# Kernel optimization log

Hardware: AMD Instinct MI355X
Metric: run time of the kernel (lower is better)

The kernel has to match this reference:

```python
import jax, jax.numpy as jnp
import numpy as np

B, N, X_DIM, Y_DIM, H_DIM, R_DIM = 64, 512, 128, 128, 4096, 1024


def setup_inputs() -> dict:
    key = jax.random.key(0)
    ks = jax.random.split(key, 10)
    x = jax.random.normal(ks[0], (B, N, X_DIM), dtype=jnp.float32)
    y = jax.random.normal(ks[1], (B, N, Y_DIM), dtype=jnp.float32)
    # per-sample context lengths in [1, N]; prefix mask guarantees >=1 True per row
    lengths = jax.random.randint(ks[2], (B,), 1, N + 1)
    mask = (jnp.arange(N)[None, :] < lengths[:, None])  # [B, N] bool
    d_in = X_DIM + Y_DIM
    s1 = 1.0 / np.sqrt(d_in)
    s2 = 1.0 / np.sqrt(H_DIM)
    W1 = jax.random.uniform(ks[3], (d_in, H_DIM), jnp.float32, -s1, s1)
    b1 = jax.random.uniform(ks[4], (H_DIM,), jnp.float32, -s1, s1)
    W2 = jax.random.uniform(ks[5], (H_DIM, H_DIM), jnp.float32, -s2, s2)
    b2 = jax.random.uniform(ks[6], (H_DIM,), jnp.float32, -s2, s2)
    W3 = jax.random.uniform(ks[7], (H_DIM, R_DIM), jnp.float32, -s2, s2)
    b3 = jax.random.uniform(ks[8], (R_DIM,), jnp.float32, -s2, s2)
    return {"x": x, "y": y, "mask": mask,
            "W1": W1, "b1": b1, "W2": W2, "b2": b2, "W3": W3, "b3": b3}


def reference(x, y, mask, W1, b1, W2, b2, W3, b3):
    # Dense equivalent of gather -> MLP -> scatter_mean by batch id:
    # the MLP is pointwise over tokens, so applying it densely and taking a
    # masked mean over the point dim gives identical math to the ragged path.
    nn_in = jnp.concatenate([x, y], axis=-1)          # [B, N, x+y]
    h = jax.nn.relu(jnp.einsum('bnd,dh->bnh', nn_in, W1) + b1)
    h = jax.nn.relu(jnp.einsum('bnh,hk->bnk', h, W2) + b2)
    r = jnp.einsum('bnk,kr->bnr', h, W3) + b3          # [B, N, r_dim]
    m = mask.astype(r.dtype)[..., None]                # [B, N, 1]
    counts = jnp.maximum(m.sum(axis=1), 1.0)           # [B, 1]
    r_aggr = (r * m).sum(axis=1) / counts              # [B, r_dim]
    return r_aggr
```

## Files before the change

### kernel.cpp

```cpp
#include <hip/hip_runtime.h>


using u16 = unsigned short;
using u8 = unsigned char;
typedef float f32x4 __attribute__((ext_vector_type(4)));
typedef short s16x8 __attribute__((ext_vector_type(8)));
typedef int i32x4 __attribute__((ext_vector_type(4)));

__device__ __forceinline__ u16 f2bf(float f) {
  union { float f; unsigned u; } v; v.f = f;
  unsigned r = (v.u + 0x7fffu + ((v.u >> 16) & 1u)) >> 16;
  return (u16)r;
}


__global__ void count_k(const int* __restrict__ mask, int* __restrict__ lens) {
  int b = blockIdx.x, l = threadIdx.x;
  const int4* row = (const int4*)(mask + (size_t)b * 512);
  int4 v0 = row[l];
  int4 v1 = row[l + 64];
  int s = v0.x + v0.y + v0.z + v0.w + v1.x + v1.y + v1.z + v1.w;
  #pragma unroll
  for (int o = 32; o; o >>= 1) s += __shfl_down(s, o);
  if (l == 0) lens[b] = s;
}

__global__ void meta_k(const int* __restrict__ lens, int* __restrict__ meta) {
  if (threadIdx.x == 0) {
    int acc = 0; meta[0] = 0;
    for (int b = 0; b < 64; ++b) { acc += lens[b]; meta[b + 1] = acc; }
    meta[65] = acc;
    meta[66] = (acc + 127) >> 7;
  }
}

__global__ void tok2b_k(const int* __restrict__ meta, int* __restrict__ tok2b) {
  int i = blockIdx.x * 256 + threadIdx.x;
  int total = meta[65];
  int b = 64;
  if (i < total) {
    int lo = 0, hi = 64;
    while (hi - lo > 1) { int mid = (lo + hi) >> 1; if (meta[mid] <= i) lo = mid; else hi = mid; }
    b = lo;
  }
  tok2b[i] = b;
}

__global__ void build_a(const float* __restrict__ x, const float* __restrict__ y,
                        const int* __restrict__ meta, const int* __restrict__ tok2b,
                        u16* __restrict__ A) {
  int i4 = blockIdx.x * 256 + threadIdx.x;
  int e = i4 * 4;
  int m = e >> 8, c = e & 255;
  int total = meta[65];
  ushort4 o = {0, 0, 0, 0};
  if (m < total) {
    int b = tok2b[m], t = m - meta[b];
    const float* src = (c < 128) ? x + ((size_t)b * 512 + t) * 128 + c
                                 : y + ((size_t)b * 512 + t) * 128 + (c - 128);
    float4 v = *(const float4*)src;
    o.x = f2bf(v.x); o.y = f2bf(v.y); o.z = f2bf(v.z); o.w = f2bf(v.w);
  }
  *(ushort4*)&A[e] = o;
}

__global__ void pack_k(const float* __restrict__ W, u16* __restrict__ P,
                       int N, int NKB) {
  long c = (long)blockIdx.x * 256 + threadIdx.x;
  int lane = c & 63; long r = c >> 6;
  int s = r & 1; int j = (r >> 1) & 3; int wn = (r >> 3) & 1;
  long q = r >> 4;
  int ktb = (int)(q % NKB), nt = (int)(q / NKB);
  int k = ktb * 64 + s * 32 + (lane >> 4) * 8;
  int n = nt * 128 + wn * 64 + j * 16 + (lane & 15);
  ushort o[8];
  #pragma unroll
  for (int e = 0; e < 8; ++e) o[e] = f2bf(W[(size_t)(k + e) * N + n]);
  *(uint4*)&P[c * 8] = *(uint4*)o;
}

__global__ void colmax_k(const float* __restrict__ W, float* __restrict__ cmax) {
  int n = blockIdx.x * 256 + threadIdx.x;
  int k0 = blockIdx.y * 128;
  float m = 0.f;
  for (int k = k0; k < k0 + 128; ++k)
    m = fmaxf(m, fabsf(W[(size_t)k * 4096 + n]));
  atomicMax((int*)&cmax[n], __float_as_int(m));
}

__global__ void pack8_k(const float* __restrict__ W, const float* __restrict__ cmax,
                        char* __restrict__ P) {
  long c = (long)blockIdx.x * 256 + threadIdx.x;
  int lane = c & 63; long r = c >> 6;
  int j = r & 3; int wn = (r >> 2) & 1; long q = r >> 3;
  int ktb = (int)(q & 63), nt = (int)(q >> 6);
  int k = ktb * 64 + (lane >> 4) * 16;
  int n = nt * 128 + wn * 64 + j * 16 + (lane & 15);
  float rw = 127.0f / fmaxf(cmax[n], 1e-20f);
  char o[16];
  #pragma unroll
  for (int e = 0; e < 16; ++e) {
    int v = __float2int_rn(W[(size_t)(k + e) * 4096 + n] * rw);
    v = v > 127 ? 127 : (v < -127 ? -127 : v);
    o[e] = (char)v;
  }
  *(uint4*)&P[c * 16] = *(const uint4*)o;
}

__global__ void sn_k(const float* __restrict__ S, const int* __restrict__ lens,
                     u16* __restrict__ Sn) {
  int i4 = blockIdx.x * 256 + threadIdx.x;
  int e = i4 * 4;
  int m = e >> 12;
  float inv = (m < 64) ? (1.0f / (float)lens[m]) : 0.0f;
  float4 v = *(const float4*)(S + e);
  ushort4 o;
  o.x = f2bf(v.x * inv); o.y = f2bf(v.y * inv);
  o.z = f2bf(v.z * inv); o.w = f2bf(v.w * inv);
  *(ushort4*)&Sn[e] = o;
}

template <int MODE>
__global__ __launch_bounds__(256, 3) void gemm_k(
    const void* __restrict__ Av, int lda, const void* __restrict__ BPv,
    const float* __restrict__ bias, const float* __restrict__ cmax,
    u8* __restrict__ Hout, float* __restrict__ Sout, float* __restrict__ Fout,
    const int* __restrict__ meta, const int* __restrict__ tok2b,
    int K, int Nld, int tile0, int tile_cap) {
  constexpr bool A8 = (MODE == 1);
  constexpr int WC_STEADY = A8 ? 0x0F7A : 0x0F7C;
  __shared__ union {
    u16 a16[2][128 * 64];
    u8  a8[2][128 * 64];
    u8  outT8[128 * 128];
  } sm;

  const int tid = threadIdx.x;
  const int wave = tid >> 6;
  const int lane = tid & 63;
  const int wm = wave >> 1, wn = wave & 1;
  const int quad = lane >> 4, l15 = lane & 15;
  const int NKB = K >> 6;

  int nslots;
  if constexpr (MODE < 2) {
    int tc = meta[66] - tile0;
    tc = tc < 0 ? 0 : (tc > tile_cap ? tile_cap : tc);
    nslots = tc * 32;
  } else {
    nslots = gridDim.x;
  }

  for (int slot = blockIdx.x; slot < nslots; slot += gridDim.x) {
    int mt, n0, k0, kend;
    if constexpr (MODE < 2) {
      mt = slot >> 5; n0 = (slot & 31) << 7; k0 = 0; kend = K;
    } else {
      mt = 0; n0 = slot << 7; k0 = blockIdx.y * 512; kend = k0 + 512;
    }

    f32x4 accf[4][4];
    i32x4 acci[4][4];
    #pragma unroll
    for (int i = 0; i < 4; i++)
      #pragma unroll
      for (int j = 0; j < 4; j++) {
        if constexpr (A8) acci[i][j] = (i32x4){0, 0, 0, 0};
        else accf[i][j] = (f32x4){0.f, 0.f, 0.f, 0.f};
      }

    const u8* ag8[2];
    const u16* ag16[4];
    if constexpr (A8) {
      #pragma unroll
      for (int il = 0; il < 2; ++il) {
        int ci = (wave * 2 + il) * 64 + lane;
        int m = ci >> 2, c = (ci & 3) ^ ((m >> 1) & 3);
        ag8[il] = (const u8*)Av + (size_t)(mt * 128 + m) * lda + c * 16;
      }
    } else {
      #pragma unroll
      for (int il = 0; il < 4; ++il) {
        int ci = (wave * 4 + il) * 64 + lane;
        int m = ci >> 3, c = (ci & 7) ^ (m & 7);
        ag16[il] = (const u16*)Av + (size_t)(mt * 128 + m) * lda + c * 8;
      }
    }
    const u16* bw = nullptr;
    const u8* bw8 = nullptr;
    if constexpr (A8)
      bw8 = (const u8*)BPv + (size_t)(n0 >> 7) * NKB * 8192 + wn * 4096 + lane * 16;
    else
      bw = (const u16*)BPv + (size_t)(n0 >> 7) * NKB * 8192 + wn * 4096 + lane * 8;

    s16x8 breg0[8], breg1[8];
    i32x4 breg8_0[4], breg8_1[4];

    auto stageA = [&](int kt, int buf) {
      if constexpr (A8) {
        #pragma unroll
        for (int il = 0; il < 2; ++il)
          __builtin_amdgcn_global_load_lds(
              (const __attribute__((address_space(1))) void*)(ag8[il] + kt),
              (__attribute__((address_space(3))) void*)(&sm.a8[buf][(wave * 2 + il) * 1024]),
              16, 0, 0);
      } else {
        #pragma unroll
        for (int il = 0; il < 4; ++il)
          __builtin_amdgcn_global_load_lds(
              (const __attribute__((address_space(1))) void*)(ag16[il] + kt),
              (__attribute__((address_space(3))) void*)(&sm.a16[buf][(wave * 4 + il) * 512]),
              16, 0, 0);
      }
    };
    auto loadB = [&](int kt, int which) {
      if constexpr (A8) {
        i32x4* dst = which ? breg8_1 : breg8_0;
        const u8* p = bw8 + (size_t)(kt >> 6) * 8192;
        #pragma unroll
        for (int j = 0; j < 4; j++)
          dst[j] = *(const i32x4*)(p + j * 1024);
      } else {
        s16x8* dst = which ? breg1 : breg0;
        const u16* p = bw + (size_t)(kt >> 6) * 8192;
        #pragma unroll
        for (int j = 0; j < 4; j++)
          #pragma unroll
          for (int s = 0; s < 2; s++)
            dst[j * 2 + s] = *(const s16x8*)(p + j * 1024 + s * 512);
      }
    };
    auto compute = [&](int buf) {
      if constexpr (A8) {
        const i32x4* br = buf ? breg8_1 : breg8_0;
        #pragma unroll
        for (int i = 0; i < 4; i++) {
          int m = wm * 64 + i * 16 + l15;
          int addr = (m * 4 + (quad ^ ((m >> 1) & 3))) * 16;
          i32x4 a = *(const i32x4*)&sm.a8[buf][addr];
          #pragma unroll
          for (int j = 0; j < 4; j++)
            acci[i][j] = __builtin_amdgcn_mfma_i32_16x16x64_i8(
                a, br[j], acci[i][j], 0, 0, 0);
        }
      } else {
        const s16x8* br = buf ? breg1 : breg0;
        #pragma unroll
        for (int s = 0; s < 2; ++s) {
          s16x8 af[4];
          #pragma unroll
          for (int i = 0; i < 4; i++) {
            int m = wm * 64 + i * 16 + l15;
            int c = (s * 4 + quad) ^ (m & 7);
            af[i] = *(const s16x8*)&sm.a16[buf][(m * 8 + c) * 8];
          }
          #pragma unroll
          for (int i = 0; i < 4; i++)
            #pragma unroll
            for (int j = 0; j < 4; j++)
              accf[i][j] = __builtin_amdgcn_mfma_f32_16x16x32_bf16(
                  af[i], br[j * 2 + s], accf[i][j], 0, 0, 0);
        }
      }
    };

    stageA(k0, 0);
    if (k0 + 64 < kend) stageA(k0 + 64, 1);
    loadB(k0, 0);

    for (int kt = k0; kt < kend; kt += 128) {
      loadB(kt + 64, 1);
      __builtin_amdgcn_s_waitcnt(WC_STEADY);
      __builtin_amdgcn_s_barrier();
      compute(0);
      __builtin_amdgcn_s_barrier();
      if (kt + 128 < kend) stageA(kt + 128, 0);
      if (kt + 128 < kend) {
        loadB(kt + 128, 0);
        __builtin_amdgcn_s_waitcnt(WC_STEADY);
      } else {
        __builtin_amdgcn_s_waitcnt(0x0F70);
      }
      __builtin_amdgcn_s_barrier();
      compute(1);
      __builtin_amdgcn_s_barrier();
      if (kt + 192 < kend) stageA(kt + 192, 1);
    }
    __syncthreads();

    if constexpr (MODE == 0) {
      float bb[4];
      #pragma unroll
      for (int j = 0; j < 4; j++) bb[j] = bias[n0 + wn * 64 + j * 16 + l15];
      #pragma unroll
      for (int i = 0; i < 4; i++)
        #pragma unroll
        for (int j = 0; j < 4; j++) {
          int col = wn * 64 + j * 16 + l15;
          #pragma unroll
          for (int r = 0; r < 4; r++) {
            int row = wm * 64 + i * 16 + quad * 4 + r;
            float v = accf[i][j][r] + bb[j];
            v = v > 0.f ? v : 0.f;
            int qv = (int)(v * 32.0f + 0.5f);
            if (qv > 127) qv = 127;
            sm.outT8[row * 128 + col] = (u8)qv;
          }
        }
      __syncthreads();
      #pragma unroll
      for (int u = 0; u < 4; ++u) {
        int e = u * 256 + tid;
        int row = e >> 3, c16 = (e & 7) * 16;
        *(uint4*)&Hout[(size_t)(mt * 128 + row) * Nld + n0 + c16] =
            *(const uint4*)&sm.outT8[row * 128 + c16];
      }
      __syncthreads();
    } else if constexpr (MODE == 1) {
      float bb[4], sc[4];
      #pragma unroll
      for (int j = 0; j < 4; j++) {
        int col_ = n0 + wn * 64 + j * 16 + l15;
        bb[j] = bias[col_];
        sc[j] = cmax[col_] * (1.0f / (127.0f * 32.0f));
      }
      int tb[16];
      const int gbase = tile0 * 128 + mt * 128 + wm * 64 + quad * 4;
      #pragma unroll
      for (int i = 0; i < 4; i++)
        #pragma unroll
        for (int r = 0; r < 4; r++) tb[i * 4 + r] = tok2b[gbase + i * 16 + r];
      #pragma unroll
      for (int j = 0; j < 4; j++) {
        int col = n0 + wn * 64 + j * 16 + l15;
        float sum = 0.f;
        int cb = tb[0];
        #pragma unroll
        for (int idx = 0; idx < 16; ++idx) {
          float t = (float)acci[idx >> 2][j][idx & 3] * sc[j] + bb[j];
          t = t > 0.f ? t : 0.f;
          int b = tb[idx];
          if (b != cb) {
            atomicAdd(&Sout[(size_t)cb * 4096 + col], sum);
            sum = 0.f; cb = b;
          }
          sum += t;
        }
        atomicAdd(&Sout[(size_t)cb * 4096 + col], sum);
      }
    } else {
      float bb[4];
      #pragma unroll
      for (int j = 0; j < 4; j++)
        bb[j] = (blockIdx.y == 0) ? bias[n0 + wn * 64 + j * 16 + l15] : 0.f;
      #pragma unroll
      for (int i = 0; i < 4; i++)
        #pragma unroll
        for (int j = 0; j < 4; j++) {
          int col = wn * 64 + j * 16 + l15;
          #pragma unroll
          for (int r = 0; r < 4; r++) {
            int row = wm * 64 + i * 16 + quad * 4 + r;
            if (row < 64)
              atomicAdd(&Fout[(size_t)row * Nld + n0 + col], accf[i][j][r] + bb[j]);
          }
        }
    }
  }
}

extern "C" void kernel_launch(void* const* d_in, const int* in_sizes, int n_in,
                              void* d_out, int out_size, void* d_ws, size_t ws_size,
                              hipStream_t stream) {
  const float* x  = (const float*)d_in[0];
  const float* y  = (const float*)d_in[1];
  const int* mask = (const int*)d_in[2];
  const float* W1 = (const float*)d_in[3];
  const float* b1 = (const float*)d_in[4];
  const float* W2 = (const float*)d_in[5];
  const float* b2 = (const float*)d_in[6];
  const float* W3 = (const float*)d_in[7];
  const float* b3 = (const float*)d_in[8];
  float* out = (float*)d_out;

  char* ws = (char*)d_ws;
  size_t off = 0;
  auto alloc = [&](size_t bytes) {
    char* p = ws + off;
    off += (bytes + 255) & ~(size_t)255;
    return p;
  };
  int* lens  = (int*)alloc(64 * 4);
  int* meta  = (int*)alloc(70 * 4);
  int* tok2b = (int*)alloc((size_t)32768 * 4);
  float* S   = (float*)alloc((size_t)128 * 4096 * 4);
  u16* Sn    = (u16*)alloc((size_t)128 * 4096 * 2);
  float* cm  = (float*)alloc((size_t)4096 * 4);
  u16* W1P   = (u16*)alloc((size_t)256 * 4096 * 2);
  char* W2P8 = (char*)alloc((size_t)4096 * 4096);
  u16* W3P   = (u16*)alloc((size_t)4096 * 1024 * 2);
  u16* Abuf  = (u16*)alloc((size_t)32768 * 256 * 2);
  size_t fixed = off;
  size_t h1_full = (size_t)32768 * 4096;
  int nchunks, tile_cap;
  if (ws_size >= fixed + h1_full) { nchunks = 1; tile_cap = 256; }
  else if (ws_size >= fixed + h1_full / 2) { nchunks = 2; tile_cap = 128; }
  else if (ws_size >= fixed + h1_full / 4) { nchunks = 4; tile_cap = 64; }
  else return;
  u8* H1 = (u8*)alloc(h1_full / nchunks);

  hipMemsetAsync(S, 0, (size_t)128 * 4096 * 4, stream);
  hipMemsetAsync(cm, 0, (size_t)4096 * 4, stream);
  hipMemsetAsync(out, 0, (size_t)out_size * 4, stream);
  count_k<<<64, 64, 0, stream>>>(mask, lens);
  meta_k<<<1, 64, 0, stream>>>(lens, meta);
  tok2b_k<<<128, 256, 0, stream>>>(meta, tok2b);
  build_a<<<8192, 256, 0, stream>>>(x, y, meta, tok2b, Abuf);
  pack_k<<<512, 256, 0, stream>>>(W1, W1P, 4096, 4);
  colmax_k<<<dim3(16, 32), 256, 0, stream>>>(W2, cm);
  pack8_k<<<4096, 256, 0, stream>>>(W2, cm, W2P8);
  pack_k<<<2048, 256, 0, stream>>>(W3, W3P, 1024, 64);

  for (int c = 0; c < nchunks; ++c) {
    gemm_k<0><<<dim3(768), 256, 0, stream>>>(
        Abuf + (size_t)c * tile_cap * 128 * 256, 256, W1P, b1, nullptr, H1,
        nullptr, nullptr, meta, tok2b, 256, 4096, c * tile_cap, tile_cap);
    gemm_k<1><<<dim3(768), 256, 0, stream>>>(
        H1, 4096, W2P8, b2, cm, nullptr, S, nullptr,
        meta, tok2b, 4096, 4096, c * tile_cap, tile_cap);
  }
  sn_k<<<512, 256, 0, stream>>>(S, lens, Sn);
  gemm_k<2><<<dim3(8, 8), 256, 0, stream>>>(
      Sn, 4096, W3P, b3, nullptr, nullptr, nullptr, out,
      meta, tok2b, 4096, 1024, 0, 0);
}
```

Baseline: 632.3 us.

## Double int8 GEMM K-tile to 128 per stage with 8-chunk swizzle

```diff
diff --git a/kernel.cpp b/kernel.cpp
--- a/kernel.cpp
+++ b/kernel.cpp
@@ -128,10 +128,11 @@
     const int* __restrict__ meta, const int* __restrict__ tok2b,
     int K, int Nld, int tile0, int tile_cap) {
   constexpr bool A8 = (MODE == 1);
-  constexpr int WC_STEADY = A8 ? 0x0F7A : 0x0F7C;
+  constexpr int KSTEP = A8 ? 256 : 128;
+  constexpr int HALF = KSTEP / 2;
   __shared__ union {
     u16 a16[2][128 * 64];
-    u8  a8[2][128 * 64];
+    u8  a8[2][128 * 128];
     u8  outT8[128 * 128];
   } sm;
 
@@ -169,13 +170,13 @@
         else accf[i][j] = (f32x4){0.f, 0.f, 0.f, 0.f};
       }
 
-    const u8* ag8[2];
+    const u8* ag8[4];
     const u16* ag16[4];
     if constexpr (A8) {
       #pragma unroll
-      for (int il = 0; il < 2; ++il) {
-        int ci = (wave * 2 + il) * 64 + lane;
-        int m = ci >> 2, c = (ci & 3) ^ ((m >> 1) & 3);
+      for (int il = 0; il < 4; ++il) {
+        int ci = (wave * 4 + il) * 64 + lane;
+        int m = ci >> 3, c = (ci & 7) ^ (m & 7);
         ag8[il] = (const u8*)Av + (size_t)(mt * 128 + m) * lda + c * 16;
       }
     } else {
@@ -194,15 +195,15 @@
       bw = (const u16*)BPv + (size_t)(n0 >> 7) * NKB * 8192 + wn * 4096 + lane * 8;
 
     s16x8 breg0[8], breg1[8];
-    i32x4 breg8_0[4], breg8_1[4];
+    i32x4 breg8_0[8], breg8_1[8];
 
     auto stageA = [&](int kt, int buf) {
       if constexpr (A8) {
         #pragma unroll
-        for (int il = 0; il < 2; ++il)
+        for (int il = 0; il < 4; ++il)
           __builtin_amdgcn_global_load_lds(
               (const __attribute__((address_space(1))) void*)(ag8[il] + kt),
-              (__attribute__((address_space(3))) void*)(&sm.a8[buf][(wave * 2 + il) * 1024]),
+              (__attribute__((address_space(3))) void*)(&sm.a8[buf][(wave * 4 + il) * 1024]),
               16, 0, 0);
       } else {
         #pragma unroll
@@ -218,8 +219,10 @@
         i32x4* dst = which ? breg8_1 : breg8_0;
         const u8* p = bw8 + (size_t)(kt >> 6) * 8192;
         #pragma unroll
-        for (int j = 0; j < 4; j++)
-          dst[j] = *(const i32x4*)(p + j * 1024);
+        for (int s = 0; s < 2; s++)
+          #pragma unroll
+          for (int j = 0; j < 4; j++)
+            dst[s * 4 + j] = *(const i32x4*)(p + s * 8192 + j * 1024);
       } else {
         s16x8* dst = which ? breg1 : breg0;
         const u16* p = bw + (size_t)(kt >> 6) * 8192;
@@ -234,14 +237,17 @@
       if constexpr (A8) {
         const i32x4* br = buf ? breg8_1 : breg8_0;
         #pragma unroll
-        for (int i = 0; i < 4; i++) {
-          int m = wm * 64 + i * 16 + l15;
-          int addr = (m * 4 + (quad ^ ((m >> 1) & 3))) * 16;
-          i32x4 a = *(const i32x4*)&sm.a8[buf][addr];
-          #pragma unroll
-          for (int j = 0; j < 4; j++)
-            acci[i][j] = __builtin_amdgcn_mfma_i32_16x16x64_i8(
-                a, br[j], acci[i][j], 0, 0, 0);
+        for (int s = 0; s < 2; ++s) {
+          #pragma unroll
+          for (int i = 0; i < 4; i++) {
+            int m = wm * 64 + i * 16 + l15;
+            int c = (s * 4 + quad) ^ (m & 7);
+            i32x4 a = *(const i32x4*)&sm.a8[buf][(m * 8 + c) * 16];
+            #pragma unroll
+            for (int j = 0; j < 4; j++)
+              acci[i][j] = __builtin_amdgcn_mfma_i32_16x16x64_i8(
+                  a, br[s * 4 + j], acci[i][j], 0, 0, 0);
+          }
         }
       } else {
         const s16x8* br = buf ? breg1 : breg0;
@@ -265,26 +271,26 @@
     };
 
     stageA(k0, 0);
-    if (k0 + 64 < kend) stageA(k0 + 64, 1);
+    if (k0 + HALF < kend) stageA(k0 + HALF, 1);
     loadB(k0, 0);
 
-    for (int kt = k0; kt < kend; kt += 128) {
-      loadB(kt + 64, 1);
-      __builtin_amdgcn_s_waitcnt(WC_STEADY);
+    for (int kt = k0; kt < kend; kt += KSTEP) {
+      loadB(kt + HALF, 1);
+      __builtin_amdgcn_s_waitcnt(0x0F7C);
       __builtin_amdgcn_s_barrier();
       compute(0);
       __builtin_amdgcn_s_barrier();
-      if (kt + 128 < kend) stageA(kt + 128, 0);
-      if (kt + 128 < kend) {
-        loadB(kt + 128, 0);
-        __builtin_amdgcn_s_waitcnt(WC_STEADY);
+      if (kt + KSTEP < kend) stageA(kt + KSTEP, 0);
+      if (kt + KSTEP < kend) {
+        loadB(kt + KSTEP, 0);
+        __builtin_amdgcn_s_waitcnt(0x0F7C);
       } else {
         __builtin_amdgcn_s_waitcnt(0x0F70);
       }
       __builtin_amdgcn_s_barrier();
       compute(1);
       __builtin_amdgcn_s_barrier();
-      if (kt + 192 < kend) stageA(kt + 192, 1);
+      if (kt + KSTEP + HALF < kend) stageA(kt + KSTEP + HALF, 1);
     }
     __syncthreads();
 
```

New measurement: 607.4 us. -3.9%, faster.
